# Kernel tuning notes

Measured on AMD Instinct MI355X. Metric: run time of the kernel, lower is better.

Reference implementation:

```python
import jax, jax.numpy as jnp
import numpy as np

K = 8                     # block_size
EPS_MIN, EPS_MAX = 2.0, 15.0
ROUND_M, ROUND_N = 10, 10
TEMP = 50.0               # round_temperature
INIT_QUALITY = 90

STD_LUMA = np.array([[16,11,10,16,24,40,51,61],[12,12,14,19,26,58,60,55],[14,13,16,24,40,57,69,56],[14,17,22,29,51,87,80,62],[18,22,37,56,68,109,103,77],[24,35,55,64,81,104,113,92],[49,64,78,87,103,121,120,101],[72,92,95,98,112,100,103,99]], dtype=np.float32)
STD_CHROMA = np.array([[17,18,24,47,99,99,99,99],[18,21,26,66,99,99,99,99],[24,26,56,99,99,99,99,99],[47,66,99,99,99,99,99,99],[99,99,99,99,99,99,99,99],[99,99,99,99,99,99,99,99],[99,99,99,99,99,99,99,99],[99,99,99,99,99,99,99,99]], dtype=np.float32)

def _quality_to_table(base, quality):
    scale = 5000.0 / quality if quality < 50 else 200.0 - 2.0 * quality
    return np.clip(np.floor((base * scale + 50.0) / 100.0), 1.0, 255.0).astype(np.float32)

def _dct_matrix(k):
    n = np.arange(k)
    mat = np.sqrt(2.0 / k) * np.cos((2 * n[None, :] + 1) * n[:, None] * np.pi / (2.0 * k))
    mat[0, :] = np.sqrt(1.0 / k)
    return jnp.asarray(mat, dtype=jnp.float32)

DCT = _dct_matrix(K)  # (K, K)

def _soft_round(x):
    # Differentiable staircase round over integer range [-M, N]:
    # round(x) ~= -M + sum_{k=-M}^{N-1} sigmoid(T * (x - k - 0.5))
    ks = jnp.arange(-ROUND_M, ROUND_N, dtype=jnp.float32)
    return -float(ROUND_M) + jnp.sum(jax.nn.sigmoid(TEMP * (x[..., None] - ks - 0.5)), axis=-1)

def setup_inputs() -> dict:
    key = jax.random.key(0)
    k_img, _ = jax.random.split(key)
    images = jax.random.uniform(k_img, (8, 3, 512, 512), dtype=jnp.float32)
    q_y = jnp.asarray(_quality_to_table(STD_LUMA, INIT_QUALITY))
    q_c = jnp.asarray(_quality_to_table(STD_CHROMA, INIT_QUALITY))
    return {"images": images, "q_y": q_y, "q_c": q_c}

def reference(images, q_y, q_c):
    x = jnp.clip(images, 0.0, 1.0)
    B, C, H, W = x.shape  # H, W are multiples of K (no padding needed)
    # RGB -> YCbCr
    r, g, b = x[:, 0:1], x[:, 1:2], x[:, 2:3]
    y  =  0.299 * r + 0.587 * g + 0.114 * b
    cb = -0.168736 * r - 0.331264 * g + 0.5 * b + 0.5
    cr =  0.5 * r - 0.418688 * g - 0.081312 * b + 0.5
    yc = jnp.concatenate([y, cb, cr], axis=1)
    # blockwise layout: (B, C, H/K, W/K, K, K)
    blocks = yc.reshape(B, C, H // K, K, W // K, K).transpose(0, 1, 2, 4, 3, 5)
    # 2D DCT per original code convention: coef = D @ X @ D (note: NOT D X D^T)
    coef = jnp.einsum('ij,bcuvjk,kl->bcuvil', DCT, blocks, DCT)
    # clamped learnable quant tables; chroma table shared by Cb and Cr
    qy = jnp.clip(q_y, EPS_MIN, EPS_MAX)
    qc = jnp.clip(q_c, EPS_MIN, EPS_MAX)
    qt = jnp.stack([qy, qc, qc])[None, :, None, None]  # (1,3,1,1,K,K)
    quant = _soft_round(coef / qt) * qt
    # 2D IDCT: rec = D^T @ X @ D^T (inverse of the above convention)
    rec = jnp.einsum('ji,bcuvjk,lk->bcuvil', DCT, quant, DCT)
    rec = rec.transpose(0, 1, 2, 4, 3, 5).reshape(B, C, H, W)
    # YCbCr -> RGB
    y2, cb2, cr2 = rec[:, 0:1], rec[:, 1:2] - 0.5, rec[:, 2:3] - 0.5
    r2 = y2 + 1.402 * cr2
    g2 = y2 - 0.344136 * cb2 - 0.714136 * cr2
    b2 = y2 + 1.772 * cb2
    out = jnp.concatenate([r2, g2, b2], axis=1)
    return jnp.clip(out, 0.0, 1.0)
```

## Files before the change

kernel.cpp:

```cpp
#include <hip/hip_runtime.h>
#include <math.h>

namespace {

constexpr int LDSS = 76;

struct DctMat {
  float d[8][8];
  constexpr DctMat() : d{} {
    const float CT[17] = {
        1.0f, 0.9807852804032304f, 0.9238795325112867f, 0.8314696123025452f,
        0.7071067811865476f, 0.5555702330196022f, 0.3826834323650898f,
        0.19509032201612825f, 0.0f, -0.19509032201612825f,
        -0.3826834323650898f, -0.5555702330196022f, -0.7071067811865476f,
        -0.8314696123025452f, -0.9238795325112867f, -0.9807852804032304f,
        -1.0f};
    for (int i = 0; i < 8; ++i)
      for (int j = 0; j < 8; ++j) {
        if (i == 0) {
          d[i][j] = 0.35355339059327373f;
        } else {
          int m = ((2 * j + 1) * i) % 32;
          if (m > 16) m = 32 - m;
          d[i][j] = 0.5f * CT[m];
        }
      }
  }
};
constexpr DctMat DM{};

template <bool TRANSPOSED>
__device__ __forceinline__ void mul8(const float (&a)[8], float (&t)[8]) {
#pragma unroll
  for (int i = 0; i < 8; ++i) {
    float s = 0.0f;
#pragma unroll
    for (int j = 0; j < 8; ++j) {
      s = fmaf(a[j], TRANSPOSED ? DM.d[j][i] : DM.d[i][j], s);
    }
    t[i] = s;
  }
}

__device__ __forceinline__ void transpose8(float (&a)[8], float* lp, int r) {
#pragma unroll
  for (int j = 0; j < 8; ++j) lp[j * 8 + r] = a[j];
  __syncthreads();
#pragma unroll
  for (int h = 0; h < 2; ++h) {
    float4 v = *reinterpret_cast<const float4*>(lp + r * 8 + h * 4);
    a[h * 4 + 0] = v.x;
    a[h * 4 + 1] = v.y;
    a[h * 4 + 2] = v.z;
    a[h * 4 + 3] = v.w;
  }
}

__device__ __forceinline__ void process_chan(float (&a)[8], const float (&qcol)[8],
                                             float* lp, int r) {
  float t[8];
  mul8<true>(a, t);
  transpose8(t, lp, r);
  mul8<false>(t, a);
#pragma unroll
  for (int i = 0; i < 8; ++i) {
    float qv = qcol[i];
    float x = a[i] * __builtin_amdgcn_rcpf(qv);
    float kc = floorf(x);
    kc = fmaxf(-10.0f, fminf(9.0f, kc));
    float arg = 50.0f * (x - kc - 0.5f);
    float e = __expf(-arg);
    float sr = kc + __builtin_amdgcn_rcpf(1.0f + e);
    a[i] = sr * qv;
  }
  mul8<true>(a, t);
  transpose8(t, lp, r);
  mul8<false>(t, a);
}

__device__ __forceinline__ void load8(const float* __restrict__ p, float (&a)[8]) {
  float4 v0 = *reinterpret_cast<const float4*>(p);
  float4 v1 = *reinterpret_cast<const float4*>(p + 4);
  a[0] = v0.x; a[1] = v0.y; a[2] = v0.z; a[3] = v0.w;
  a[4] = v1.x; a[5] = v1.y; a[6] = v1.z; a[7] = v1.w;
}

__device__ __forceinline__ void store8(float* __restrict__ p, const float (&a)[8]) {
  float4 v0 = {a[0], a[1], a[2], a[3]};
  float4 v1 = {a[4], a[5], a[6], a[7]};
  *reinterpret_cast<float4*>(p) = v0;
  *reinterpret_cast<float4*>(p + 4) = v1;
}

__global__ __launch_bounds__(256) void jpeg_kernel(
    const float* __restrict__ img, const float* __restrict__ qy,
    const float* __restrict__ qc, float* __restrict__ out) {
  __shared__ float lds[4 * 8 * LDSS];

  const int tid = threadIdx.x;
  const int wave = tid >> 6;
  const int lane = tid & 63;
  const int blk = lane & 7;
  const int r = lane >> 3;

  const int w = blockIdx.x * 4 + wave;
  const int b = w >> 9;
  const int rr = w & 511;
  const int u = rr >> 3;
  const int v0 = (rr & 7) << 3;

  const int row = u * 8 + r;
  const int col = (v0 + blk) * 8;

  float* lp = lds + (wave * 8 + blk) * LDSS;

  const size_t ims = 512 * 512;
  const float* pbase = img + (size_t)b * 3 * ims + (size_t)row * 512 + col;

  float R[8], G[8], B[8];
  load8(pbase, R);
  load8(pbase + ims, G);
  load8(pbase + 2 * ims, B);

  float qycol[8], qccol[8];
#pragma unroll
  for (int i = 0; i < 8; ++i) {
    qycol[i] = fminf(fmaxf(qy[i * 8 + r], 2.0f), 15.0f);
    qccol[i] = fminf(fmaxf(qc[i * 8 + r], 2.0f), 15.0f);
  }

  float Y[8], Cb[8], Cr[8];
#pragma unroll
  for (int i = 0; i < 8; ++i) {
    float rv = fminf(fmaxf(R[i], 0.0f), 1.0f);
    float gv = fminf(fmaxf(G[i], 0.0f), 1.0f);
    float bv = fminf(fmaxf(B[i], 0.0f), 1.0f);
    Y[i] = 0.299f * rv + 0.587f * gv + 0.114f * bv;
    Cb[i] = -0.168736f * rv - 0.331264f * gv + 0.5f * bv + 0.5f;
    Cr[i] = 0.5f * rv - 0.418688f * gv - 0.081312f * bv + 0.5f;
  }

  process_chan(Y, qycol, lp, r);
  process_chan(Cb, qccol, lp, r);
  process_chan(Cr, qccol, lp, r);

  float R2[8], G2[8], B2[8];
#pragma unroll
  for (int i = 0; i < 8; ++i) {
    float y2 = Y[i];
    float cb2 = Cb[i] - 0.5f;
    float cr2 = Cr[i] - 0.5f;
    float r2 = y2 + 1.402f * cr2;
    float g2 = y2 - 0.344136f * cb2 - 0.714136f * cr2;
    float b2 = y2 + 1.772f * cb2;
    R2[i] = fminf(fmaxf(r2, 0.0f), 1.0f);
    G2[i] = fminf(fmaxf(g2, 0.0f), 1.0f);
    B2[i] = fminf(fmaxf(b2, 0.0f), 1.0f);
  }

  float* obase = out + (size_t)b * 3 * ims + (size_t)row * 512 + col;
  store8(obase, R2);
  store8(obase + ims, G2);
  store8(obase + 2 * ims, B2);
}

}

extern "C" void kernel_launch(void* const* d_in, const int* in_sizes, int n_in,
                              void* d_out, int out_size, void* d_ws, size_t ws_size,
                              hipStream_t stream) {
  const float* img = (const float*)d_in[0];
  const float* qy = (const float*)d_in[1];
  const float* qc = (const float*)d_in[2];
  float* out = (float*)d_out;
  jpeg_kernel<<<dim3(1024), dim3(256), 0, stream>>>(img, qy, qc, out);
}
```

Before: 82.88 us.

## Batch YCbCr channel transposes and launch single-wave workgroups

Runs the DCT row pass for all three channels, then does one shared LDS transpose for all of them before the column pass. The same is done for the inverse DCT, cutting block-wide barriers from six to two and exposing more independent arithmetic per thread. Workgroups shrink from four waves to one wave, so each barrier only synchronises a single wave, and the grid grows to match. The cost is higher register pressure from keeping three channels' worth of temporaries live, plus an added trailing barrier that guards LDS reuse.

```diff
diff --git a/kernel.cpp b/kernel.cpp
--- a/kernel.cpp
+++ b/kernel.cpp
@@ -42,29 +42,30 @@
   }
 }
 
-__device__ __forceinline__ void transpose8(float (&a)[8], float* lp, int r) {
+__device__ __forceinline__ void transpose3(float (&T)[3][8], float* lds, int blk,
+                                           int r) {
 #pragma unroll
-  for (int j = 0; j < 8; ++j) lp[j * 8 + r] = a[j];
+  for (int c = 0; c < 3; ++c) {
+    float* lp = lds + (c * 8 + blk) * LDSS;
+#pragma unroll
+    for (int j = 0; j < 8; ++j) lp[j * 8 + r] = T[c][j];
+  }
   __syncthreads();
 #pragma unroll
-  for (int h = 0; h < 2; ++h) {
-    float4 v = *reinterpret_cast<const float4*>(lp + r * 8 + h * 4);
-    a[h * 4 + 0] = v.x;
-    a[h * 4 + 1] = v.y;
-    a[h * 4 + 2] = v.z;
-    a[h * 4 + 3] = v.w;
+  for (int c = 0; c < 3; ++c) {
+    const float* lp = lds + (c * 8 + blk) * LDSS + r * 8;
+    float4 v0 = *reinterpret_cast<const float4*>(lp);
+    float4 v1 = *reinterpret_cast<const float4*>(lp + 4);
+    T[c][0] = v0.x; T[c][1] = v0.y; T[c][2] = v0.z; T[c][3] = v0.w;
+    T[c][4] = v1.x; T[c][5] = v1.y; T[c][6] = v1.z; T[c][7] = v1.w;
   }
+  __syncthreads();
 }
 
-__device__ __forceinline__ void process_chan(float (&a)[8], const float (&qcol)[8],
-                                             float* lp, int r) {
-  float t[8];
-  mul8<true>(a, t);
-  transpose8(t, lp, r);
-  mul8<false>(t, a);
+__device__ __forceinline__ void quant8(float (&a)[8], const float (&q)[8]) {
 #pragma unroll
   for (int i = 0; i < 8; ++i) {
-    float qv = qcol[i];
+    float qv = q[i];
     float x = a[i] * __builtin_amdgcn_rcpf(qv);
     float kc = floorf(x);
     kc = fmaxf(-10.0f, fminf(9.0f, kc));
@@ -73,9 +74,6 @@
     float sr = kc + __builtin_amdgcn_rcpf(1.0f + e);
     a[i] = sr * qv;
   }
-  mul8<true>(a, t);
-  transpose8(t, lp, r);
-  mul8<false>(t, a);
 }
 
 __device__ __forceinline__ void load8(const float* __restrict__ p, float (&a)[8]) {
@@ -92,18 +90,16 @@
   *reinterpret_cast<float4*>(p + 4) = v1;
 }
 
-__global__ __launch_bounds__(256) void jpeg_kernel(
+__global__ __launch_bounds__(64) void jpeg_kernel(
     const float* __restrict__ img, const float* __restrict__ qy,
     const float* __restrict__ qc, float* __restrict__ out) {
-  __shared__ float lds[4 * 8 * LDSS];
+  __shared__ float lds[3 * 8 * LDSS];
 
-  const int tid = threadIdx.x;
-  const int wave = tid >> 6;
-  const int lane = tid & 63;
+  const int lane = threadIdx.x;
   const int blk = lane & 7;
   const int r = lane >> 3;
 
-  const int w = blockIdx.x * 4 + wave;
+  const int w = blockIdx.x;
   const int b = w >> 9;
   const int rr = w & 511;
   const int u = rr >> 3;
@@ -111,8 +107,6 @@
 
   const int row = u * 8 + r;
   const int col = (v0 + blk) * 8;
-
-  float* lp = lds + (wave * 8 + blk) * LDSS;
 
   const size_t ims = 512 * 512;
   const float* pbase = img + (size_t)b * 3 * ims + (size_t)row * 512 + col;
@@ -129,27 +123,40 @@
     qccol[i] = fminf(fmaxf(qc[i * 8 + r], 2.0f), 15.0f);
   }
 
-  float Y[8], Cb[8], Cr[8];
+  float A[3][8];
 #pragma unroll
   for (int i = 0; i < 8; ++i) {
     float rv = fminf(fmaxf(R[i], 0.0f), 1.0f);
     float gv = fminf(fmaxf(G[i], 0.0f), 1.0f);
     float bv = fminf(fmaxf(B[i], 0.0f), 1.0f);
-    Y[i] = 0.299f * rv + 0.587f * gv + 0.114f * bv;
-    Cb[i] = -0.168736f * rv - 0.331264f * gv + 0.5f * bv + 0.5f;
-    Cr[i] = 0.5f * rv - 0.418688f * gv - 0.081312f * bv + 0.5f;
+    A[0][i] = 0.299f * rv + 0.587f * gv + 0.114f * bv;
+    A[1][i] = -0.168736f * rv - 0.331264f * gv + 0.5f * bv + 0.5f;
+    A[2][i] = 0.5f * rv - 0.418688f * gv - 0.081312f * bv + 0.5f;
   }
 
-  process_chan(Y, qycol, lp, r);
-  process_chan(Cb, qccol, lp, r);
-  process_chan(Cr, qccol, lp, r);
+  float T[3][8];
+#pragma unroll
+  for (int c = 0; c < 3; ++c) mul8<true>(A[c], T[c]);
+  transpose3(T, lds, blk, r);
+#pragma unroll
+  for (int c = 0; c < 3; ++c) mul8<false>(T[c], A[c]);
+
+  quant8(A[0], qycol);
+  quant8(A[1], qccol);
+  quant8(A[2], qccol);
+
+#pragma unroll
+  for (int c = 0; c < 3; ++c) mul8<true>(A[c], T[c]);
+  transpose3(T, lds, blk, r);
+#pragma unroll
+  for (int c = 0; c < 3; ++c) mul8<false>(T[c], A[c]);
 
   float R2[8], G2[8], B2[8];
 #pragma unroll
   for (int i = 0; i < 8; ++i) {
-    float y2 = Y[i];
-    float cb2 = Cb[i] - 0.5f;
-    float cr2 = Cr[i] - 0.5f;
+    float y2 = A[0][i];
+    float cb2 = A[1][i] - 0.5f;
+    float cr2 = A[2][i] - 0.5f;
     float r2 = y2 + 1.402f * cr2;
     float g2 = y2 - 0.344136f * cb2 - 0.714136f * cr2;
     float b2 = y2 + 1.772f * cb2;
@@ -173,5 +180,5 @@
   const float* qy = (const float*)d_in[1];
   const float* qc = (const float*)d_in[2];
   float* out = (float*)d_out;
-  jpeg_kernel<<<dim3(1024), dim3(256), 0, stream>>>(img, qy, qc, out);
+  jpeg_kernel<<<dim3(4096), dim3(64), 0, stream>>>(img, qy, qc, out);
 }
```

Result: no change. 81.98 us (-1.1%).
